# Performance work log

Hardware: AMD Instinct MI355X
Metric: run time of the kernel (lower is better)

Reference implementation:

```python
import jax, jax.numpy as jnp
import numpy as np

DIM = 1024
H = 16
HKV = 4
HD = DIM // H  # 64
GROUP = H // HKV
ROPE_BASE = 10000.0
B, T = 2, 2048


def rms_norm(x, eps):
    return x * jax.lax.rsqrt(jnp.mean(x * x, axis=-1, keepdims=True) + eps)


def apply_rotary(x, cos, sin):
    # x: [B, h, T, HD]; cos/sin: [1, 1, T, HD//2]
    half = x.shape[-1] // 2
    x1, x2 = x[..., :half], x[..., half:]
    return jnp.concatenate([x1 * cos + x2 * sin, -x1 * sin + x2 * cos], axis=-1)


def setup_inputs() -> dict:
    key = jax.random.key(0)
    ks = jax.random.split(key, 5)
    s = 0.02
    return {
        "x": jax.random.normal(ks[0], (B, T, DIM), dtype=jnp.float32),
        "Wq": jax.random.normal(ks[1], (DIM, DIM), dtype=jnp.float32) * s,
        "Wk": jax.random.normal(ks[2], (HKV * HD, DIM), dtype=jnp.float32) * s,
        "Wv": jax.random.normal(ks[3], (HKV * HD, DIM), dtype=jnp.float32) * s,
        "Wproj": jax.random.normal(ks[4], (DIM, DIM), dtype=jnp.float32) * s,
        "q_gain": jnp.full((H,), 12.0, dtype=jnp.float32),
    }


def reference(x, Wq, Wk, Wv, Wproj, q_gain):
    bsz, seqlen, dim = x.shape
    eps = jnp.asarray(jnp.finfo(x.dtype).eps, x.dtype)

    # double RMSNorm path: normalized input for q/k, raw input for v
    x_qk = rms_norm(x, eps)
    q = (x_qk @ Wq.T).reshape(bsz, seqlen, H, HD).transpose(0, 2, 1, 3)    # [B,H,T,D]
    k = (x_qk @ Wk.T).reshape(bsz, seqlen, HKV, HD).transpose(0, 2, 1, 3)  # [B,Hkv,T,D]
    v = (x @ Wv.T).reshape(bsz, seqlen, HKV, HD).transpose(0, 2, 1, 3)     # [B,Hkv,T,D]

    q = rms_norm(q, eps)
    k = rms_norm(k, eps)

    # rotary embeddings
    t = jnp.arange(seqlen, dtype=jnp.float32)
    inv_freq = 1.0 / (ROPE_BASE ** (jnp.arange(0, HD, 2, dtype=jnp.float32) / HD))
    freqs = jnp.outer(t, inv_freq)                       # [T, HD//2]
    cos = jnp.cos(freqs)[None, None].astype(x.dtype)
    sin = jnp.sin(freqs)[None, None].astype(x.dtype)
    q = apply_rotary(q, cos, sin)
    k = apply_rotary(k, cos, sin)

    # per-head gain on q
    q = q * q_gain.astype(q.dtype)[None, :, None, None]

    # GQA: expand kv heads to query heads
    k_r = jnp.repeat(k, GROUP, axis=1)  # [B,H,T,D]
    v_r = jnp.repeat(v, GROUP, axis=1)

    scale = 1.0 / np.sqrt(HD)
    scores = jnp.einsum("bhqd,bhkd->bhqk", q, k_r) * scale
    causal = jnp.tril(jnp.ones((seqlen, seqlen), dtype=bool))
    scores = jnp.where(causal[None, None], scores, jnp.asarray(-jnp.inf, scores.dtype))
    attn = jax.nn.softmax(scores, axis=-1)
    y = jnp.einsum("bhqk,bhkd->bhqd", attn, v_r)          # [B,H,T,D]

    # XSA: remove value-direction component from output
    y_bt = y.transpose(0, 2, 1, 3)                        # [B,T,H,D]
    v_bt = v.transpose(0, 2, 1, 3)                        # [B,T,Hkv,D]
    y_g = y_bt.reshape(bsz, seqlen, HKV, GROUP, HD)
    vnorm = jnp.sqrt(jnp.sum(v_bt * v_bt, axis=-1, keepdims=True))
    vn = (v_bt / jnp.maximum(vnorm, 1e-12))[..., None, :]  # [B,T,Hkv,1,D]
    proj = jnp.sum(y_g * vn, axis=-1, keepdims=True) * vn
    y_bt = (y_g - proj).reshape(bsz, seqlen, H, HD)

    return y_bt.reshape(bsz, seqlen, dim) @ Wproj.T
```

## Files before the change

kernel.cpp:

```cpp
#include <hip/hip_runtime.h>
#include <hip/hip_bf16.h>

typedef __attribute__((ext_vector_type(8))) short bf8v;
typedef __attribute__((ext_vector_type(4))) float f4v;

#define MFMA16(a,b,c) __builtin_amdgcn_mfma_f32_16x16x32_bf16((a),(b),(c),0,0,0)

#define GLD16(gp, lp) __builtin_amdgcn_global_load_lds( \
    (const __attribute__((address_space(1))) void*)(gp), \
    (__attribute__((address_space(3))) void*)(lp), 16, 0, 0)

#define DIMC   1024
#define TSEQ   2048
#define NH     16
#define NKV    4
#define HDIM   64
#define RMS_EPS 1.1920929e-07f
#define QSCALE 0.1803368801111601f

__device__ __forceinline__ ushort f2bf(float f) {
  unsigned u = __builtin_bit_cast(unsigned, f);
  u = (u + 0x7FFFu + ((u >> 16) & 1u)) >> 16;
  return (ushort)u;
}
__device__ __forceinline__ float bf2f(ushort u) {
  return __builtin_bit_cast(float, (unsigned)u << 16);
}
__device__ __forceinline__ unsigned cvtpk(float lo, float hi) {
  unsigned r;
  asm("v_cvt_pk_bf16_f32 %0, %1, %2" : "=v"(r) : "v"(lo), "v"(hi));
  return r;
}

__global__ __launch_bounds__(256) void prep_all(
    const float* __restrict__ x,
    const float* __restrict__ Wq, const float* __restrict__ Wk,
    const float* __restrict__ Wv, const float* __restrict__ Wp,
    ushort* __restrict__ xhi, ushort* __restrict__ xlo,
    ushort* __restrict__ xb,
    ushort* __restrict__ wqkh, ushort* __restrict__ wqkl,
    ushort* __restrict__ wvb, ushort* __restrict__ wpb,
    float* __restrict__ cosT, float* __restrict__ sinT) {
  __shared__ float red[4];
  int bid = blockIdx.x, tid = threadIdx.x;
  if (bid < 4096) {
    int row = bid;
    int lane = tid & 63, w = tid >> 6;
    float4 v = ((const float4*)(x + (size_t)row * DIMC))[tid];
    float ss = v.x * v.x + v.y * v.y + v.z * v.z + v.w * v.w;
    for (int off = 32; off; off >>= 1) ss += __shfl_xor(ss, off);
    if (lane == 0) red[w] = ss;
    __syncthreads();
    float tot = red[0] + red[1] + red[2] + red[3];
    float rs = rsqrtf(tot * (1.0f / DIMC) + RMS_EPS);
    float n0 = v.x * rs, n1 = v.y * rs, n2 = v.z * rs, n3 = v.w * rs;
    ushort4 h, l, ob;
    h.x = f2bf(n0); l.x = f2bf(n0 - bf2f(h.x));
    h.y = f2bf(n1); l.y = f2bf(n1 - bf2f(h.y));
    h.z = f2bf(n2); l.z = f2bf(n2 - bf2f(h.z));
    h.w = f2bf(n3); l.w = f2bf(n3 - bf2f(h.w));
    ob.x = f2bf(v.x); ob.y = f2bf(v.y); ob.z = f2bf(v.z); ob.w = f2bf(v.w);
    ((ushort4*)(xhi + (size_t)row * DIMC))[tid] = h;
    ((ushort4*)(xlo + (size_t)row * DIMC))[tid] = l;
    ((ushort4*)(xb  + (size_t)row * DIMC))[tid] = ob;
    return;
  }
  int wb = bid - 4096;
  if (wb < 1280) {
    const float* src;
    size_t si, di;
    if (wb < 1024) { src = Wq; si = (size_t)wb * 256 + tid; di = si; }
    else { src = Wk; si = (size_t)(wb - 1024) * 256 + tid; di = 262144 + si; }
    float4 v = ((const float4*)src)[si];
    ushort4 h, l;
    h.x = f2bf(v.x); l.x = f2bf(v.x - bf2f(h.x));
    h.y = f2bf(v.y); l.y = f2bf(v.y - bf2f(h.y));
    h.z = f2bf(v.z); l.z = f2bf(v.z - bf2f(h.z));
    h.w = f2bf(v.w); l.w = f2bf(v.w - bf2f(h.w));
    ((ushort4*)wqkh)[di] = h;
    ((ushort4*)wqkl)[di] = l;
  } else if (wb < 2560) {
    const float* src;
    ushort* dst;
    int i;
    if (wb < 1536) { src = Wv; dst = wvb; i = (wb - 1280) * 256 + tid; }
    else           { src = Wp; dst = wpb; i = (wb - 1536) * 256 + tid; }
    float4 v = ((const float4*)src)[i];
    ushort4 o;
    o.x = f2bf(v.x); o.y = f2bf(v.y); o.z = f2bf(v.z); o.w = f2bf(v.w);
    ((ushort4*)dst)[i] = o;
  } else {
    int i = (wb - 2560) * 256 + tid;
    int t = i >> 5, j = i & 31;
    float inv = 1.0f / powf(10000.0f, (float)j * (1.0f / 32.0f));
    float f = (float)t * inv;
    cosT[i] = cosf(f);
    sinT[i] = sinf(f);
  }
}

__global__ __launch_bounds__(256, 3)
void gemm_qkv(const ushort* __restrict__ xhi, const ushort* __restrict__ xlo,
              const ushort* __restrict__ wqkh, const ushort* __restrict__ wqkl,
              float* __restrict__ QKf, ushort* __restrict__ QKc,
              const ushort* __restrict__ xb, const ushort* __restrict__ wvb,
              float* __restrict__ Vf) {
  __shared__ __align__(16) ushort lA[128 * 64];
  __shared__ __align__(16) ushort lB[128 * 64];
  const int bid = blockIdx.x;
  int u;
  bool big;
  if (bid < 256)      { big = true;  u = bid; }
  else if (bid < 448) { big = false; u = bid - 256; }
  else if (bid < 512) { big = true;  u = 256 + (bid - 448); }
  else                { big = false; u = 192 + (bid - 512); }

  const ushort *Ap0, *Bp0, *Ap1, *Bp1;
  float* Cf = QKf;
  int N = 1280, nsteps, mt, n0;
  if (big) {
    mt = u / 10; n0 = (u % 10) * 128;
    Ap0 = xlo; Bp0 = wqkh; Ap1 = xhi; Bp1 = wqkl; nsteps = 32;
  } else if (u < 320) {
    mt = u / 10; n0 = (u % 10) * 128;
    Ap0 = xhi; Bp0 = wqkh; Ap1 = Ap0; Bp1 = Bp0; nsteps = 16;
  } else {
    int v = u - 320; mt = v >> 1; n0 = (v & 1) * 128;
    Ap0 = xb; Bp0 = wvb; Ap1 = Ap0; Bp1 = Bp0; nsteps = 16;
    Cf = Vf; N = 256;
  }
  const int m0 = mt * 128;

  const int t = threadIdx.x;
  const int lane = t & 63, w = t >> 6;
  const int wr = w >> 1, wc = w & 1;
  const int l15 = lane & 15, lg = lane >> 4;
  const int srow = t >> 3, scp = t & 7;

  f4v acc[4][4] = {};

  for (int s = 0; s < nsteps; ++s) {
    const ushort* Ab = (s < 16) ? Ap0 : Ap1;
    const ushort* Bb = (s < 16) ? Bp0 : Bp1;
    const int kk = (s & 15) * 64;
    for (int i = 0; i < 4; ++i) {
      int row = srow + i * 32;
      int sc = scp ^ (row & 7);
      const ushort* ga = Ab + (size_t)(m0 + row) * DIMC + kk + sc * 8;
      const ushort* gb = Bb + (size_t)(n0 + row) * DIMC + kk + sc * 8;
      GLD16(ga, &lA[w * 512 + i * 2048]);
      GLD16(gb, &lB[w * 512 + i * 2048]);
    }
    __syncthreads();
    for (int kx = 0; kx < 2; ++kx) {
      bf8v af[4], bfr[4];
      for (int m = 0; m < 4; ++m) {
        int row = wr * 64 + m * 16 + l15;
        int ch = (kx * 4 + lg) ^ (row & 7);
        af[m] = *(const bf8v*)&lA[row * 64 + ch * 8];
      }
      for (int n = 0; n < 4; ++n) {
        int row = wc * 64 + n * 16 + l15;
        int ch = (kx * 4 + lg) ^ (row & 7);
        bfr[n] = *(const bf8v*)&lB[row * 64 + ch * 8];
      }
      for (int m = 0; m < 4; ++m)
        for (int n = 0; n < 4; ++n)
          acc[m][n] = MFMA16(af[m], bfr[n], acc[m][n]);
    }
    __syncthreads();
  }

  if (big) {
    for (int m = 0; m < 4; ++m)
      for (int n = 0; n < 4; ++n)
        for (int j = 0; j < 4; ++j) {
          int r = m0 + wr * 64 + m * 16 + lg * 4 + j;
          int c = n0 + wc * 64 + n * 16 + l15;
          QKc[(size_t)r * 1280 + c] = f2bf(acc[m][n][j]);
        }
  } else {
    for (int m = 0; m < 4; ++m)
      for (int n = 0; n < 4; ++n)
        for (int j = 0; j < 4; ++j) {
          int r = m0 + wr * 64 + m * 16 + lg * 4 + j;
          int c = n0 + wc * 64 + n * 16 + l15;
          Cf[(size_t)r * N + c] = acc[m][n][j];
        }
  }
}

__global__ __launch_bounds__(256, 2)
void gemm_bt(const ushort* __restrict__ A0, const ushort* __restrict__ B0,
             float* __restrict__ C, int N) {
  __shared__ __align__(16) ushort lA[128 * 64];
  __shared__ __align__(16) ushort lB[128 * 64];
  const int t = threadIdx.x;
  const int lane = t & 63, w = t >> 6;
  const int wr = w >> 1, wc = w & 1;
  const int l15 = lane & 15, lg = lane >> 4;
  const int m0 = blockIdx.y * 128, n0 = blockIdx.x * 128;
  const int srow = t >> 3, scp = t & 7;

  f4v acc[4][4] = {};

  for (int k0 = 0; k0 < 1024; k0 += 64) {
    for (int i = 0; i < 4; ++i) {
      int row = srow + i * 32;
      int sc = scp ^ (row & 7);
      const ushort* ga = A0 + (size_t)(m0 + row) * DIMC + k0 + sc * 8;
      const ushort* gb = B0 + (size_t)(n0 + row) * DIMC + k0 + sc * 8;
      GLD16(ga, &lA[w * 512 + i * 2048]);
      GLD16(gb, &lB[w * 512 + i * 2048]);
    }
    __syncthreads();
    for (int kx = 0; kx < 2; ++kx) {
      bf8v af[4], bfr[4];
      for (int m = 0; m < 4; ++m) {
        int row = wr * 64 + m * 16 + l15;
        int ch = (kx * 4 + lg) ^ (row & 7);
        af[m] = *(const bf8v*)&lA[row * 64 + ch * 8];
      }
      for (int n = 0; n < 4; ++n) {
        int row = wc * 64 + n * 16 + l15;
        int ch = (kx * 4 + lg) ^ (row & 7);
        bfr[n] = *(const bf8v*)&lB[row * 64 + ch * 8];
      }
      for (int m = 0; m < 4; ++m)
        for (int n = 0; n < 4; ++n)
          acc[m][n] = MFMA16(af[m], bfr[n], acc[m][n]);
    }
    __syncthreads();
  }

  for (int m = 0; m < 4; ++m)
    for (int n = 0; n < 4; ++n)
      for (int j = 0; j < 4; ++j) {
        int r = m0 + wr * 64 + m * 16 + lg * 4 + j;
        int c = n0 + wc * 64 + n * 16 + l15;
        C[(size_t)r * N + c] = acc[m][n][j];
      }
}

__global__ __launch_bounds__(256) void post_all(
    const float* __restrict__ QKf, const ushort* __restrict__ QKc,
    const float* __restrict__ cosT,
    const float* __restrict__ sinT, const float* __restrict__ qgain,
    ushort* __restrict__ qhi, ushort* __restrict__ qlo,
    ushort* __restrict__ kb16,
    const float* __restrict__ Vf, ushort* __restrict__ vt2,
    ushort* __restrict__ vhat_t) {
  __shared__ float lds[64][69];
  __shared__ float rnv[64];
  int bid = blockIdx.x;
  if (bid < 4096) {
    int m = bid;
    int b = m >> 11, tpos = m & 2047;
    int lane = threadIdx.x & 63, w = threadIdx.x >> 6;
    int d = lane, j = d & 31;
    float sgn = (d < 32) ? 1.0f : -1.0f;
    float c = cosT[tpos * 32 + j], s = sinT[tpos * 32 + j];

    for (int i = 0; i < 4; ++i) {
      int h = w * 4 + i;
      size_t base = (size_t)m * 1280 + h * HDIM + d;
      float q = QKf[base] + bf2f(QKc[base]);
      float ss = q * q;
      for (int off = 32; off; off >>= 1) ss += __shfl_xor(ss, off);
      float rs = rsqrtf(ss * (1.0f / HDIM) + RMS_EPS);
      float qn = q * rs;
      float partner = __shfl_xor(qn, 32);
      float ro = (qn * c + sgn * partner * s) * (qgain[h] * QSCALE);
      ushort hi = f2bf(ro);
      ushort lo = f2bf(ro - bf2f(hi));
      size_t idx = (((size_t)b * NH + h) * TSEQ + tpos) * HDIM + d;
      qhi[idx] = hi;
      qlo[idx] = lo;
    }
    {
      int kv = w;
      size_t base = (size_t)m * 1280 + 1024 + kv * HDIM + d;
      float k = QKf[base] + bf2f(QKc[base]);
      float ss = k * k;
      for (int off = 32; off; off >>= 1) ss += __shfl_xor(ss, off);
      float rs = rsqrtf(ss * (1.0f / HDIM) + RMS_EPS);
      float kn = k * rs;
      float partner = __shfl_xor(kn, 32);
      float ro = kn * c + sgn * partner * s;
      kb16[((size_t)(b * NKV + kv) * TSEQ + tpos) * HDIM + d] = f2bf(ro);
    }
    return;
  }
  {
    int vb = bid - 4096;
    int bkv = vb >> 5, tt = vb & 31;
    int b = bkv >> 2, kv = bkv & 3;
    int tid = threadIdx.x;
    for (int i = 0; i < 16; ++i) {
      int idx = i * 256 + tid;
      int tloc = idx >> 6, d = idx & 63;
      lds[d][tloc] = Vf[((size_t)(b * TSEQ + tt * 64 + tloc)) * 256 + kv * 64 + d];
    }
    __syncthreads();
    {
      int t = tid >> 2, prt = tid & 3;
      float ssum = 0.f;
      for (int dd = 0; dd < 16; ++dd) {
        float v = lds[prt * 16 + dd][t];
        ssum += v * v;
      }
      ssum += __shfl_xor(ssum, 1);
      ssum += __shfl_xor(ssum, 2);
      if (prt == 0) rnv[t] = 1.0f / fmaxf(sqrtf(ssum), 1e-12f);
    }
    __syncthreads();
    for (int i = 0; i < 16; ++i) {
      int idx = i * 256 + tid;
      int d = idx >> 6, tloc = idx & 63;
      float v = lds[d][tloc];
      vt2[(size_t)bkv * (TSEQ * 64) + tt * 4096 + d * 64 + tloc] = f2bf(v);
      vhat_t[(size_t)bkv * (TSEQ * 64) + (size_t)d * TSEQ + tt * 64 + tloc] = f2bf(v * rnv[tloc]);
    }
  }
}

__global__ __launch_bounds__(256, 4) void attn_kern(
    const ushort* __restrict__ qhi, const ushort* __restrict__ qlo,
    const ushort* __restrict__ kb16, const ushort* __restrict__ vt2,
    const ushort* __restrict__ vhat_t, ushort* __restrict__ ytil) {
  __shared__ __align__(16) ushort lk[2][64 * 64];
  __shared__ __align__(16) ushort lv[2][64 * 64];
  __shared__ __align__(16) unsigned pl[4][512];
  const int t = threadIdx.x;
  const int lane = t & 63, w = t >> 6;
  const int bid = blockIdx.x;
  const int xcd = bid & 7, g = (bid >> 3) & 3, trank = bid >> 5;
  const int ta = trank & 7, tq = trank >> 3;
  const int tile = (tq == 0) ? (31 - ta)
                 : (tq == 1) ? ta
                 : (tq == 2) ? (23 - ta)
                             : (8 + ta);
  const int b = xcd >> 2, kv = xcd & 3, h = kv * 4 + g;
  const int l15 = lane & 15, lg = lane >> 4;
  const int q0 = tile * 64 + w * 16;
  const int ntile = tile + 1;
  const int t3 = t >> 3, tc8 = t & 7;
  const int rx = l15 & 7;
  const int pswz = rx << 2;

  const size_t qoff = (((size_t)(b * NH + h)) * TSEQ + q0 + l15) * HDIM;
  bf8v bq0h = *(const bf8v*)(qhi + qoff + lg * 8);
  bf8v bq1h = *(const bf8v*)(qhi + qoff + 32 + lg * 8);
  bf8v bq0l = *(const bf8v*)(qlo + qoff + lg * 8);
  bf8v bq1l = *(const bf8v*)(qlo + qoff + 32 + lg * 8);

  const ushort* kb = kb16 + (size_t)(b * NKV + kv) * TSEQ * 64;
  const ushort* vb = vt2 + (size_t)(b * NKV + kv) * TSEQ * 64;
  unsigned* pw = &pl[w][0];

#define STAGE(BUF, IT) do { \
    _Pragma("unroll") \
    for (int i = 0; i < 2; ++i) { \
      int row = i * 32 + t3; \
      int sc = tc8 ^ (row & 7); \
      GLD16(kb + (size_t)((IT) * 64 + row) * 64 + sc * 8, \
            &lk[BUF][(i * 32 + (w << 3)) * 64]); \
      GLD16(vb + (size_t)(IT) * 4096 + row * 64 + sc * 8, \
            &lv[BUF][(i * 32 + (w << 3)) * 64]); \
    } } while (0)

  STAGE(0, 0);

  f4v y[4] = {};
  float mrow = -1e30f, lrow = 0.f;

#pragma unroll 1
  for (int it = 0; it < ntile; ++it) {
    const int cur = it & 1;
    __syncthreads();
    if (it + 1 < ntile) STAGE(cur ^ 1, it + 1);

    const ushort* lkc = &lk[cur][0];
    const ushort* lvc = &lv[cur][0];
    const int kv0 = it * 64;

    f4v s[4];
    __builtin_amdgcn_s_setprio(1);
#pragma unroll
    for (int n = 0; n < 4; ++n) {
      const ushort* krow = lkc + (n * 16 + l15) * 64;
      bf8v kh0 = *(const bf8v*)&krow[((0 + lg) ^ rx) * 8];
      bf8v kh1 = *(const bf8v*)&krow[((4 + lg) ^ rx) * 8];
      f4v z = {};
      f4v acc = MFMA16(kh0, bq0h, z);
      acc = MFMA16(kh1, bq1h, acc);
      acc = MFMA16(kh0, bq0l, acc);
      acc = MFMA16(kh1, bq1l, acc);
      s[n] = acc;
    }
    __builtin_amdgcn_s_setprio(0);

    const bool need_mask = (it == ntile - 1);
    float mloc = -1e30f;
#pragma unroll
    for (int n = 0; n < 4; ++n)
#pragma unroll
      for (int j = 0; j < 4; ++j) {
        float v = s[n][j];
        if (need_mask && (kv0 + n * 16 + lg * 4 + j > q0 + l15)) v = -1e30f;
        s[n][j] = v;
        mloc = fmaxf(mloc, v);
      }
    mloc = fmaxf(mloc, __shfl_xor(mloc, 16));
    mloc = fmaxf(mloc, __shfl_xor(mloc, 32));
    if (__any(mloc > mrow + 11.5f)) {
      float mnew = fmaxf(mrow, mloc);
      float scf = exp2f(mrow - mnew);
      lrow *= scf;
#pragma unroll
      for (int n = 0; n < 4; ++n) y[n] *= scf;
      mrow = mnew;
    }
    float rs = 0.f;
#pragma unroll
    for (int n = 0; n < 4; ++n)
#pragma unroll
      for (int j = 0; j < 4; ++j) {
        float e = exp2f(s[n][j] - mrow);
        s[n][j] = e;
        rs += e;
      }
    rs += __shfl_xor(rs, 16);
    rs += __shfl_xor(rs, 32);
    lrow += rs;

#pragma unroll
    for (int n = 0; n < 4; ++n) {
      uint2 pk;
      pk.x = cvtpk(s[n][0], s[n][1]);
      pk.y = cvtpk(s[n][2], s[n][3]);
      *(uint2*)&pw[l15 * 32 + ((8 * n + 2 * lg) ^ pswz)] = pk;
    }
    asm volatile("s_waitcnt lgkmcnt(0)" ::: "memory");
    bf8v pb0 = *(const bf8v*)&pw[l15 * 32 + ((lg * 4) ^ pswz)];
    bf8v pb1 = *(const bf8v*)&pw[l15 * 32 + ((16 + lg * 4) ^ pswz)];
    __builtin_amdgcn_s_setprio(1);
#pragma unroll
    for (int n = 0; n < 4; ++n) {
      const ushort* vrow = lvc + (n * 16 + l15) * 64;
      bf8v va0 = *(const bf8v*)&vrow[((0 + lg) ^ rx) * 8];
      bf8v va1 = *(const bf8v*)&vrow[((4 + lg) ^ rx) * 8];
      y[n] = MFMA16(va0, pb0, y[n]);
      y[n] = MFMA16(va1, pb1, y[n]);
    }
    __builtin_amdgcn_s_setprio(0);
  }
#undef STAGE

  {
    float inv = 1.0f / lrow;
    const ushort* vh = vhat_t + (size_t)(b * NKV + kv) * TSEQ * 64;
    ushort* yw = (ushort*)pw;
    float vv[4][4];
    float dp = 0.f;
#pragma unroll
    for (int n = 0; n < 4; ++n)
#pragma unroll
      for (int j = 0; j < 4; ++j) {
        int d = n * 16 + lg * 4 + j;
        float yv = y[n][j] * inv;
        y[n][j] = yv;
        vv[n][j] = bf2f(vh[(size_t)d * TSEQ + q0 + l15]);
        dp += yv * vv[n][j];
      }
    dp += __shfl_xor(dp, 16);
    dp += __shfl_xor(dp, 32);
#pragma unroll
    for (int n = 0; n < 4; ++n)
#pragma unroll
      for (int j = 0; j < 4; ++j) {
        int d = n * 16 + lg * 4 + j;
        yw[l15 * 64 + (((d >> 3) ^ rx) << 3) + (d & 7)] = f2bf(y[n][j] - dp * vv[n][j]);
      }
    asm volatile("s_waitcnt lgkmcnt(0)" ::: "memory");
    int row = lane >> 2, quad = lane & 3;
    bf8v y0 = *(const bf8v*)(yw + row * 64 + ((quad ^ (row & 7)) << 3));
    bf8v y1 = *(const bf8v*)(yw + row * 64 + (((quad + 4) ^ (row & 7)) << 3));
    size_t gbase = ((size_t)(b * TSEQ + q0 + row)) * DIMC + h * HDIM + quad * 8;
    *(bf8v*)(ytil + gbase) = y0;
    *(bf8v*)(ytil + gbase + 32) = y1;
  }
}

extern "C" void kernel_launch(void* const* d_in, const int* in_sizes, int n_in,
                              void* d_out, int out_size, void* d_ws, size_t ws_size,
                              hipStream_t stream) {
  (void)in_sizes; (void)n_in; (void)out_size; (void)ws_size;
  const float* x  = (const float*)d_in[0];
  const float* Wq = (const float*)d_in[1];
  const float* Wk = (const float*)d_in[2];
  const float* Wv = (const float*)d_in[3];
  const float* Wp = (const float*)d_in[4];
  const float* qg = (const float*)d_in[5];
  float* out = (float*)d_out;
  char* ws = (char*)d_ws;
  const size_t KB = 1024, MB = 1ull << 20;

  ushort* xhi = (ushort*)(ws);
  ushort* xlo = (ushort*)(ws + 8 * MB);
  ushort* xb  = (ushort*)(ws + 16 * MB);
  ushort* wqkh = (ushort*)(ws + 24 * MB);
  ushort* wqkl = (ushort*)(ws + 26 * MB + 512 * KB);
  ushort* wvb = (ushort*)(ws + 29 * MB);
  ushort* wpb = (ushort*)(ws + 29 * MB + 512 * KB);
  float*  cosT = (float*)(ws + 31 * MB + 512 * KB);
  float*  sinT = (float*)(ws + 31 * MB + 768 * KB);
  float*  QKf  = (float*)(ws + 32 * MB);
  ushort* kb16 = (ushort*)(ws + 52 * MB);
  ushort* vt2  = (ushort*)(ws + 54 * MB);
  ushort* vhat = (ushort*)(ws + 56 * MB);

  float*  Vf   = out;
  ushort* QKc  = (ushort*)((char*)out + 4 * MB);
  ushort* qhb  = xhi;
  ushort* qlb  = xlo;
  ushort* ytil = xb;

  prep_all<<<6912, 256, 0, stream>>>(x, Wq, Wk, Wv, Wp, xhi, xlo, xb,
                                     wqkh, wqkl, wvb, wpb, cosT, sinT);

  gemm_qkv<<<704, 256, 0, stream>>>(xhi, xlo, wqkh, wqkl, QKf, QKc,
                                    xb, wvb, Vf);

  post_all<<<4352, 256, 0, stream>>>(QKf, QKc, cosT, sinT, qg, qhb, qlb, kb16,
                                     Vf, vt2, vhat);
  attn_kern<<<1024, 256, 0, stream>>>(qhb, qlb, kb16, vt2, vhat, ytil);
  gemm_bt<<<dim3(8, 32), 256, 0, stream>>>(ytil, wpb, out, 1024);
}
```

Before: 143.6 us.

## Split attention into 32-row query blocks and reuse K buffer for P staging

Attention blocks shrink from 256 to 128 threads, each covering 32 query rows. The grid doubles to 2048 blocks, scheduled in descending order of causal work for finer load balance. The separate P staging array is removed: the probabilities are staged in the current K shared-memory tile after an added barrier, which frees shared memory. Row-sum shuffles are deferred to the epilogue, and the row-max shuffles only run when a rescale is needed. The cost is that each K/V tile is loaded for half as many queries, so global and L2 traffic per query goes up, plus one extra barrier per iteration.

```diff
diff --git a/kernel.cpp b/kernel.cpp
--- a/kernel.cpp
+++ b/kernel.cpp
@@ -324,26 +324,21 @@
   }
 }
 
-__global__ __launch_bounds__(256, 4) void attn_kern(
+__global__ __launch_bounds__(128, 2) void attn_kern(
     const ushort* __restrict__ qhi, const ushort* __restrict__ qlo,
     const ushort* __restrict__ kb16, const ushort* __restrict__ vt2,
     const ushort* __restrict__ vhat_t, ushort* __restrict__ ytil) {
   __shared__ __align__(16) ushort lk[2][64 * 64];
   __shared__ __align__(16) ushort lv[2][64 * 64];
-  __shared__ __align__(16) unsigned pl[4][512];
   const int t = threadIdx.x;
   const int lane = t & 63, w = t >> 6;
   const int bid = blockIdx.x;
-  const int xcd = bid & 7, g = (bid >> 3) & 3, trank = bid >> 5;
-  const int ta = trank & 7, tq = trank >> 3;
-  const int tile = (tq == 0) ? (31 - ta)
-                 : (tq == 1) ? ta
-                 : (tq == 2) ? (23 - ta)
-                             : (8 + ta);
+  const int xcd = bid & 7, g = (bid >> 3) & 3, rank = bid >> 5;
+  const int tile32 = 63 - rank;
   const int b = xcd >> 2, kv = xcd & 3, h = kv * 4 + g;
   const int l15 = lane & 15, lg = lane >> 4;
-  const int q0 = tile * 64 + w * 16;
-  const int ntile = tile + 1;
+  const int q0 = tile32 * 32 + w * 16;
+  const int ntile = (tile32 >> 1) + 1;
   const int t3 = t >> 3, tc8 = t & 7;
   const int rx = l15 & 7;
   const int pswz = rx << 2;
@@ -356,17 +351,16 @@
 
   const ushort* kb = kb16 + (size_t)(b * NKV + kv) * TSEQ * 64;
   const ushort* vb = vt2 + (size_t)(b * NKV + kv) * TSEQ * 64;
-  unsigned* pw = &pl[w][0];
 
 #define STAGE(BUF, IT) do { \
     _Pragma("unroll") \
-    for (int i = 0; i < 2; ++i) { \
-      int row = i * 32 + t3; \
+    for (int i = 0; i < 4; ++i) { \
+      int row = i * 16 + t3; \
       int sc = tc8 ^ (row & 7); \
       GLD16(kb + (size_t)((IT) * 64 + row) * 64 + sc * 8, \
-            &lk[BUF][(i * 32 + (w << 3)) * 64]); \
+            &lk[BUF][(i * 16 + (w << 3)) * 64]); \
       GLD16(vb + (size_t)(IT) * 4096 + row * 64 + sc * 8, \
-            &lv[BUF][(i * 32 + (w << 3)) * 64]); \
+            &lv[BUF][(i * 16 + (w << 3)) * 64]); \
     } } while (0)
 
   STAGE(0, 0);
@@ -382,6 +376,7 @@
 
     const ushort* lkc = &lk[cur][0];
     const ushort* lvc = &lv[cur][0];
+    unsigned* pw = (unsigned*)&lk[cur][w << 10];
     const int kv0 = it * 64;
 
     f4v s[4];
@@ -411,28 +406,27 @@
         s[n][j] = v;
         mloc = fmaxf(mloc, v);
       }
-    mloc = fmaxf(mloc, __shfl_xor(mloc, 16));
-    mloc = fmaxf(mloc, __shfl_xor(mloc, 32));
     if (__any(mloc > mrow + 11.5f)) {
-      float mnew = fmaxf(mrow, mloc);
+      float mf = fmaxf(mloc, __shfl_xor(mloc, 16));
+      mf = fmaxf(mf, __shfl_xor(mf, 32));
+      float mnew = fmaxf(mrow, mf);
       float scf = exp2f(mrow - mnew);
       lrow *= scf;
 #pragma unroll
       for (int n = 0; n < 4; ++n) y[n] *= scf;
       mrow = mnew;
     }
-    float rs = 0.f;
 #pragma unroll
     for (int n = 0; n < 4; ++n)
 #pragma unroll
       for (int j = 0; j < 4; ++j) {
         float e = exp2f(s[n][j] - mrow);
         s[n][j] = e;
-        rs += e;
-      }
-    rs += __shfl_xor(rs, 16);
-    rs += __shfl_xor(rs, 32);
-    lrow += rs;
+        lrow += e;
+      }
+
+    asm volatile("s_waitcnt lgkmcnt(0)" ::: "memory");
+    __builtin_amdgcn_s_barrier();
 
 #pragma unroll
     for (int n = 0; n < 4; ++n) {
@@ -458,9 +452,12 @@
 #undef STAGE
 
   {
+    lrow += __shfl_xor(lrow, 16);
+    lrow += __shfl_xor(lrow, 32);
     float inv = 1.0f / lrow;
+    const int lastcur = (ntile - 1) & 1;
+    ushort* yw = (ushort*)&lk[lastcur][w << 10];
     const ushort* vh = vhat_t + (size_t)(b * NKV + kv) * TSEQ * 64;
-    ushort* yw = (ushort*)pw;
     float vv[4][4];
     float dp = 0.f;
 #pragma unroll
@@ -534,6 +531,6 @@
 
   post_all<<<4352, 256, 0, stream>>>(QKf, QKc, cosT, sinT, qg, qhb, qlb, kb16,
                                      Vf, vt2, vhat);
-  attn_kern<<<1024, 256, 0, stream>>>(qhb, qlb, kb16, vt2, vhat, ytil);
+  attn_kern<<<2048, 128, 0, stream>>>(qhb, qlb, kb16, vt2, vhat, ytil);
   gemm_bt<<<dim3(8, 32), 256, 0, stream>>>(ytil, wpb, out, 1024);
 }
```

New measurement: 155.1 us. 8.0% more time.
